# Kernel tuning notes

Measured on AMD Instinct MI355X. Metric: run time of the kernel, lower is better.

## Reference

```python
import jax, jax.numpy as jnp
import numpy as np

EPSILON = 0.0

def setup_inputs() -> dict:
    key = jax.random.key(0)
    k1, k2, k3, k4, k5 = jax.random.split(key, 5)
    N, MAX_NB, D_IN, D_OUT, N_BONDS = 50000, 16, 256, 256, 400000
    x = jax.random.normal(k1, (N, D_IN), dtype=jnp.float32)
    W = jax.random.normal(k2, (D_OUT, D_IN), dtype=jnp.float32) * (1.0 / np.sqrt(D_IN))
    b = jax.random.normal(k3, (D_OUT,), dtype=jnp.float32) * 0.01
    b_from_a = jax.random.randint(k4, (N_BONDS,), 0, N, dtype=jnp.int32)
    a_from_b = jax.random.randint(k5, (N, MAX_NB), 0, N_BONDS, dtype=jnp.int32)
    return {"x": x, "W": W, "b": b, "b_from_a": b_from_a, "a_from_b": a_from_b}

def reference(x, W, b, b_from_a, a_from_b):
    # a2a[i, k] = source atom of the k-th neighbor bond of atom i
    a2a = b_from_a[a_from_b]                      # [N, max_nb]
    h = x @ W.T + b                               # [N, d_out]
    h = h.at[0].set(0.0)                          # row 0 is padding
    message = h[a2a]                              # [N, max_nb, d_out] gather
    out = (1.0 + EPSILON) * h + jnp.sum(message, axis=1)
    return jax.nn.relu(out)
```

## Files before the change

### kernel.cpp

```cpp
#include <hip/hip_runtime.h>

typedef short bf16x8 __attribute__((ext_vector_type(8)));
typedef float f32x4  __attribute__((ext_vector_type(4)));

__device__ __forceinline__ unsigned short f32_to_bf16(float f) {
  union { float f; unsigned int u; } v; v.f = f;
  unsigned int u = v.u;
  u += 0x7fffu + ((u >> 16) & 1u);
  return (unsigned short)(u >> 16);
}
__device__ __forceinline__ float bf16lo_to_f32(unsigned int u) {
  union { unsigned int u; float f; } v; v.u = u << 16; return v.f;
}
__device__ __forceinline__ float bf16hi_to_f32(unsigned int u) {
  union { unsigned int u; float f; } v; v.u = u & 0xffff0000u; return v.f;
}

__global__ __launch_bounds__(256, 2) void gin_gemm(
    const float* __restrict__ x, const float* __restrict__ W,
    const float* __restrict__ bias, unsigned short* __restrict__ h, int M) {
  __shared__ __align__(16) unsigned short As[64 * 32];
  __shared__ __align__(16) unsigned short Bs[256 * 32];

  const int tid  = threadIdx.x;
  const int wid  = tid >> 6;
  const int lane = tid & 63;
  const int row0 = blockIdx.x * 64;

  f32x4 acc[4][4] = {};

  const int srow = tid >> 2;
  const int sk0  = (tid & 3) << 3;
  int agrow = row0 + srow;
  if (agrow >= M) agrow = M - 1;
  const float* aRow = x + (size_t)agrow * 256 + sk0;
  const float* bRow = W + (size_t)srow * 256 + sk0;

  for (int kt = 0; kt < 8; ++kt) {
    const int kb = kt * 32;
    {
      float4 v0 = *(const float4*)(aRow + kb);
      float4 v1 = *(const float4*)(aRow + kb + 4);
      bf16x8 u;
      u[0] = (short)f32_to_bf16(v0.x); u[1] = (short)f32_to_bf16(v0.y);
      u[2] = (short)f32_to_bf16(v0.z); u[3] = (short)f32_to_bf16(v0.w);
      u[4] = (short)f32_to_bf16(v1.x); u[5] = (short)f32_to_bf16(v1.y);
      u[6] = (short)f32_to_bf16(v1.z); u[7] = (short)f32_to_bf16(v1.w);
      *(bf16x8*)(&As[srow * 32 + sk0]) = u;
    }
#pragma unroll
    for (int j = 0; j < 4; ++j) {
      const float* p = bRow + (size_t)(j * 64) * 256 + kb;
      float4 v0 = *(const float4*)p;
      float4 v1 = *(const float4*)(p + 4);
      bf16x8 u;
      u[0] = (short)f32_to_bf16(v0.x); u[1] = (short)f32_to_bf16(v0.y);
      u[2] = (short)f32_to_bf16(v0.z); u[3] = (short)f32_to_bf16(v0.w);
      u[4] = (short)f32_to_bf16(v1.x); u[5] = (short)f32_to_bf16(v1.y);
      u[6] = (short)f32_to_bf16(v1.z); u[7] = (short)f32_to_bf16(v1.w);
      *(bf16x8*)(&Bs[(j * 64 + srow) * 32 + sk0]) = u;
    }
    __syncthreads();

    const int r16 = lane & 15;
    const int qk  = (lane >> 4) << 3;
    bf16x8 af[4], bfr[4];
#pragma unroll
    for (int g = 0; g < 4; ++g)
      af[g] = *(const bf16x8*)(&As[(g * 16 + r16) * 32 + qk]);
#pragma unroll
    for (int g = 0; g < 4; ++g)
      bfr[g] = *(const bf16x8*)(&Bs[(wid * 64 + g * 16 + r16) * 32 + qk]);
#pragma unroll
    for (int rg = 0; rg < 4; ++rg)
#pragma unroll
      for (int cg = 0; cg < 4; ++cg)
        acc[rg][cg] = __builtin_amdgcn_mfma_f32_16x16x32_bf16(
            af[rg], bfr[cg], acc[rg][cg], 0, 0, 0);
    __syncthreads();
  }

  const int quad = lane >> 4;
  const int c16  = lane & 15;
#pragma unroll
  for (int rg = 0; rg < 4; ++rg) {
#pragma unroll
    for (int r = 0; r < 4; ++r) {
      int grow = row0 + rg * 16 + quad * 4 + r;
      if (grow >= M) continue;
#pragma unroll
      for (int cg = 0; cg < 4; ++cg) {
        int col = wid * 64 + cg * 16 + c16;
        float v = acc[rg][cg][r] + bias[col];
        if (grow == 0) v = 0.0f;
        h[(size_t)grow * 256 + col] = f32_to_bf16(v);
      }
    }
  }
}

__global__ __launch_bounds__(256, 4) void gin_gather(
    const unsigned short* __restrict__ h, const int* __restrict__ b_from_a,
    const int* __restrict__ a_from_b, float* __restrict__ out, int N) {
  const int wid  = threadIdx.x >> 6;
  const int lane = threadIdx.x & 63;
  const int i = blockIdx.x * 4 + wid;
  if (i >= N) return;

  int src = 0;
  if (lane < 16) src = b_from_a[a_from_b[i * 16 + lane]];

  const int c0 = lane << 2;
  uint2 u = *(const uint2*)(h + (size_t)i * 256 + c0);
  float a0 = bf16lo_to_f32(u.x), a1 = bf16hi_to_f32(u.x);
  float a2 = bf16lo_to_f32(u.y), a3 = bf16hi_to_f32(u.y);
#pragma unroll
  for (int k = 0; k < 16; ++k) {
    int s = __shfl(src, k, 64);
    uint2 v = *(const uint2*)(h + (size_t)s * 256 + c0);
    a0 += bf16lo_to_f32(v.x); a1 += bf16hi_to_f32(v.x);
    a2 += bf16lo_to_f32(v.y); a3 += bf16hi_to_f32(v.y);
  }
  float4 r;
  r.x = fmaxf(a0, 0.0f); r.y = fmaxf(a1, 0.0f);
  r.z = fmaxf(a2, 0.0f); r.w = fmaxf(a3, 0.0f);
  *(float4*)(out + (size_t)i * 256 + c0) = r;
}

extern "C" void kernel_launch(void* const* d_in, const int* in_sizes, int n_in,
                              void* d_out, int out_size, void* d_ws, size_t ws_size,
                              hipStream_t stream) {
  const float* x        = (const float*)d_in[0];
  const float* W        = (const float*)d_in[1];
  const float* b        = (const float*)d_in[2];
  const int*   b_from_a = (const int*)d_in[3];
  const int*   a_from_b = (const int*)d_in[4];
  float*       out      = (float*)d_out;
  const int M = in_sizes[0] / 256;

  unsigned short* h = (unsigned short*)d_ws;

  gin_gemm<<<(M + 63) / 64, 256, 0, stream>>>(x, W, b, h, M);
  gin_gather<<<(M + 3) / 4, 256, 0, stream>>>(h, b_from_a, a_from_b, out, M);
}
```

Before: 191.3 us.

## Pad LDS rows, transpose GEMM output for packed stores, split gather across half-waves

The GEMM pads its shared-memory rows to a stride of 40 to reduce bank conflicts. It swaps the MFMA operand roles so each lane holds four consecutive output columns, which allows packed 8-byte bf16 stores and a bias vector hoisted into registers. The gather kernel now has each half-wave load 16-byte chunks for 8 of the 16 neighbors and combines the two halves with a cross-lane shuffle. This issues fewer, wider memory requests per neighbor row, at the cost of the extra shuffle-reduce and a split output write.

```diff
diff --git a/kernel.cpp b/kernel.cpp
--- a/kernel.cpp
+++ b/kernel.cpp
@@ -16,11 +16,13 @@
   union { unsigned int u; float f; } v; v.u = u & 0xffff0000u; return v.f;
 }
 
+#define LDSTRIDE 40
+
 __global__ __launch_bounds__(256, 2) void gin_gemm(
     const float* __restrict__ x, const float* __restrict__ W,
     const float* __restrict__ bias, unsigned short* __restrict__ h, int M) {
-  __shared__ __align__(16) unsigned short As[64 * 32];
-  __shared__ __align__(16) unsigned short Bs[256 * 32];
+  __shared__ __align__(16) unsigned short Xs[64 * LDSTRIDE];
+  __shared__ __align__(16) unsigned short Ws[256 * LDSTRIDE];
 
   const int tid  = threadIdx.x;
   const int wid  = tid >> 6;
@@ -36,6 +38,13 @@
   const float* aRow = x + (size_t)agrow * 256 + sk0;
   const float* bRow = W + (size_t)srow * 256 + sk0;
 
+  const int quad = lane >> 4;
+  const int c16  = lane & 15;
+  float4 biasv[4];
+#pragma unroll
+  for (int ng = 0; ng < 4; ++ng)
+    biasv[ng] = *(const float4*)(bias + wid * 64 + ng * 16 + quad * 4);
+
   for (int kt = 0; kt < 8; ++kt) {
     const int kb = kt * 32;
     {
@@ -46,7 +55,7 @@
       u[2] = (short)f32_to_bf16(v0.z); u[3] = (short)f32_to_bf16(v0.w);
       u[4] = (short)f32_to_bf16(v1.x); u[5] = (short)f32_to_bf16(v1.y);
       u[6] = (short)f32_to_bf16(v1.z); u[7] = (short)f32_to_bf16(v1.w);
-      *(bf16x8*)(&As[srow * 32 + sk0]) = u;
+      *(bf16x8*)(&Xs[srow * LDSTRIDE + sk0]) = u;
     }
 #pragma unroll
     for (int j = 0; j < 4; ++j) {
@@ -58,43 +67,44 @@
       u[2] = (short)f32_to_bf16(v0.z); u[3] = (short)f32_to_bf16(v0.w);
       u[4] = (short)f32_to_bf16(v1.x); u[5] = (short)f32_to_bf16(v1.y);
       u[6] = (short)f32_to_bf16(v1.z); u[7] = (short)f32_to_bf16(v1.w);
-      *(bf16x8*)(&Bs[(j * 64 + srow) * 32 + sk0]) = u;
+      *(bf16x8*)(&Ws[(j * 64 + srow) * LDSTRIDE + sk0]) = u;
     }
     __syncthreads();
 
     const int r16 = lane & 15;
     const int qk  = (lane >> 4) << 3;
-    bf16x8 af[4], bfr[4];
+    bf16x8 wf[4], xf[4];
 #pragma unroll
     for (int g = 0; g < 4; ++g)
-      af[g] = *(const bf16x8*)(&As[(g * 16 + r16) * 32 + qk]);
+      wf[g] = *(const bf16x8*)(&Ws[(wid * 64 + g * 16 + r16) * LDSTRIDE + qk]);
 #pragma unroll
     for (int g = 0; g < 4; ++g)
-      bfr[g] = *(const bf16x8*)(&Bs[(wid * 64 + g * 16 + r16) * 32 + qk]);
+      xf[g] = *(const bf16x8*)(&Xs[(g * 16 + r16) * LDSTRIDE + qk]);
 #pragma unroll
-    for (int rg = 0; rg < 4; ++rg)
+    for (int ng = 0; ng < 4; ++ng)
 #pragma unroll
-      for (int cg = 0; cg < 4; ++cg)
-        acc[rg][cg] = __builtin_amdgcn_mfma_f32_16x16x32_bf16(
-            af[rg], bfr[cg], acc[rg][cg], 0, 0, 0);
+      for (int ag = 0; ag < 4; ++ag)
+        acc[ng][ag] = __builtin_amdgcn_mfma_f32_16x16x32_bf16(
+            wf[ng], xf[ag], acc[ng][ag], 0, 0, 0);
     __syncthreads();
   }
 
-  const int quad = lane >> 4;
-  const int c16  = lane & 15;
 #pragma unroll
-  for (int rg = 0; rg < 4; ++rg) {
+  for (int ag = 0; ag < 4; ++ag) {
+    const int atom = row0 + ag * 16 + c16;
+    if (atom >= M) continue;
 #pragma unroll
-    for (int r = 0; r < 4; ++r) {
-      int grow = row0 + rg * 16 + quad * 4 + r;
-      if (grow >= M) continue;
-#pragma unroll
-      for (int cg = 0; cg < 4; ++cg) {
-        int col = wid * 64 + cg * 16 + c16;
-        float v = acc[rg][cg][r] + bias[col];
-        if (grow == 0) v = 0.0f;
-        h[(size_t)grow * 256 + col] = f32_to_bf16(v);
-      }
+    for (int ng = 0; ng < 4; ++ng) {
+      const int n0 = wid * 64 + ng * 16 + quad * 4;
+      float v0 = acc[ng][ag][0] + biasv[ng].x;
+      float v1 = acc[ng][ag][1] + biasv[ng].y;
+      float v2 = acc[ng][ag][2] + biasv[ng].z;
+      float v3 = acc[ng][ag][3] + biasv[ng].w;
+      if (atom == 0) { v0 = v1 = v2 = v3 = 0.0f; }
+      uint2 pk;
+      pk.x = (unsigned int)f32_to_bf16(v0) | ((unsigned int)f32_to_bf16(v1) << 16);
+      pk.y = (unsigned int)f32_to_bf16(v2) | ((unsigned int)f32_to_bf16(v3) << 16);
+      *(uint2*)(h + (size_t)atom * 256 + n0) = pk;
     }
   }
 }
@@ -107,24 +117,47 @@
   const int i = blockIdx.x * 4 + wid;
   if (i >= N) return;
 
+  const int half = lane >> 5;
+  const int hl   = lane & 31;
+  const int c0   = hl << 3;
+
   int src = 0;
   if (lane < 16) src = b_from_a[a_from_b[i * 16 + lane]];
 
-  const int c0 = lane << 2;
-  uint2 u = *(const uint2*)(h + (size_t)i * 256 + c0);
-  float a0 = bf16lo_to_f32(u.x), a1 = bf16hi_to_f32(u.x);
-  float a2 = bf16lo_to_f32(u.y), a3 = bf16hi_to_f32(u.y);
+  const unsigned short* hp = h + c0;
+
+  float a0, a1, a2, a3, a4, a5, a6, a7;
+  {
+    uint4 v = *(const uint4*)(hp + (size_t)i * 256);
+    const float selfw = half ? 0.0f : 1.0f;
+    a0 = selfw * bf16lo_to_f32(v.x); a1 = selfw * bf16hi_to_f32(v.x);
+    a2 = selfw * bf16lo_to_f32(v.y); a3 = selfw * bf16hi_to_f32(v.y);
+    a4 = selfw * bf16lo_to_f32(v.z); a5 = selfw * bf16hi_to_f32(v.z);
+    a6 = selfw * bf16lo_to_f32(v.w); a7 = selfw * bf16hi_to_f32(v.w);
+  }
 #pragma unroll
-  for (int k = 0; k < 16; ++k) {
-    int s = __shfl(src, k, 64);
-    uint2 v = *(const uint2*)(h + (size_t)s * 256 + c0);
+  for (int k = 0; k < 8; ++k) {
+    int s = __shfl(src, half * 8 + k, 64);
+    uint4 v = *(const uint4*)(hp + (size_t)s * 256);
     a0 += bf16lo_to_f32(v.x); a1 += bf16hi_to_f32(v.x);
     a2 += bf16lo_to_f32(v.y); a3 += bf16hi_to_f32(v.y);
+    a4 += bf16lo_to_f32(v.z); a5 += bf16hi_to_f32(v.z);
+    a6 += bf16lo_to_f32(v.w); a7 += bf16hi_to_f32(v.w);
   }
+  a0 += __shfl_xor(a0, 32, 64); a1 += __shfl_xor(a1, 32, 64);
+  a2 += __shfl_xor(a2, 32, 64); a3 += __shfl_xor(a3, 32, 64);
+  a4 += __shfl_xor(a4, 32, 64); a5 += __shfl_xor(a5, 32, 64);
+  a6 += __shfl_xor(a6, 32, 64); a7 += __shfl_xor(a7, 32, 64);
+
   float4 r;
-  r.x = fmaxf(a0, 0.0f); r.y = fmaxf(a1, 0.0f);
-  r.z = fmaxf(a2, 0.0f); r.w = fmaxf(a3, 0.0f);
-  *(float4*)(out + (size_t)i * 256 + c0) = r;
+  if (half == 0) {
+    r.x = fmaxf(a0, 0.0f); r.y = fmaxf(a1, 0.0f);
+    r.z = fmaxf(a2, 0.0f); r.w = fmaxf(a3, 0.0f);
+  } else {
+    r.x = fmaxf(a4, 0.0f); r.y = fmaxf(a5, 0.0f);
+    r.z = fmaxf(a6, 0.0f); r.w = fmaxf(a7, 0.0f);
+  }
+  *(float4*)(out + (size_t)i * 256 + c0 + half * 4) = r;
 }
 
 extern "C" void kernel_launch(void* const* d_in, const int* in_sizes, int n_in,
```

New measurement: 194.9 us. Within noise of the previous version (+1.9%).
